# Kernel tuning notes

Measured on AMD Instinct MI355X. Metric: run time of the kernel, lower is better.

## Reference

```python
import jax, jax.numpy as jnp
import numpy as np

E, H, O = 64, 128, 16  # enc_hidden_dim, dec_hidden_dim, dec_output_dim (proj_size)
B, N, FUT = 64, 1000, 12


def _lstm_proj_cell(x, h, c, W_ih, W_hh, b_ih, b_hh, W_hr):
    # PyTorch gate order: input, forget, cell(g), output
    gates = x @ W_ih.T + h @ W_hh.T + (b_ih + b_hh)
    i, f, g, o = jnp.split(gates, 4, axis=-1)
    c_new = jax.nn.sigmoid(f) * c + jax.nn.sigmoid(i) * jnp.tanh(g)
    h_full = jax.nn.sigmoid(o) * jnp.tanh(c_new)
    h_new = h_full @ W_hr.T  # proj_size projection
    return h_new, c_new


def setup_inputs() -> dict:
    key = jax.random.key(0)
    ks = jax.random.split(key, 20)
    sc = 0.1
    inp = {
        "enc_outputs": jax.random.normal(ks[0], (B, 1, N, E), jnp.float32),
        "mean": jax.random.normal(ks[1], (B, FUT, N, O), jnp.float32),
        "s": jax.random.normal(ks[2], (1, O), jnp.float32),
        "h_0": jax.random.normal(ks[3], (2, O), jnp.float32),
        "c_0": jax.random.normal(ks[4], (2, H), jnp.float32),
        "W_ih_l0": sc * jax.random.normal(ks[5], (4 * H, E + O), jnp.float32),
        "W_hh_l0": sc * jax.random.normal(ks[6], (4 * H, O), jnp.float32),
        "b_ih_l0": sc * jax.random.normal(ks[7], (4 * H,), jnp.float32),
        "b_hh_l0": sc * jax.random.normal(ks[8], (4 * H,), jnp.float32),
        "W_hr_l0": sc * jax.random.normal(ks[9], (O, H), jnp.float32),
        "W_ih_l1": sc * jax.random.normal(ks[10], (4 * H, O), jnp.float32),
        "W_hh_l1": sc * jax.random.normal(ks[11], (4 * H, O), jnp.float32),
        "b_ih_l1": sc * jax.random.normal(ks[12], (4 * H,), jnp.float32),
        "b_hh_l1": sc * jax.random.normal(ks[13], (4 * H,), jnp.float32),
        "W_hr_l1": sc * jax.random.normal(ks[14], (O, H), jnp.float32),
        "future": FUT,
    }
    # forget-gate bias = 1.0 as in reset_bias()
    for nme in ("b_ih_l0", "b_hh_l0", "b_ih_l1", "b_hh_l1"):
        inp[nme] = inp[nme].at[H:2 * H].set(1.0)
    return inp


def _forward(enc_outputs, mean, s, h_0, c_0,
             W_ih_l0, W_hh_l0, b_ih_l0, b_hh_l0, W_hr_l0,
             W_ih_l1, W_hh_l1, b_ih_l1, b_hh_l1, W_hr_l1, future):
    b, _, n_nodes, _ = enc_outputs.shape
    enc = enc_outputs[:, 0]            # [B, N, E]
    node_mean = jnp.mean(mean, axis=1)  # [B, N, O]
    # state is carried across nodes AND timesteps: one chain of N*future steps
    node_idx = jnp.arange(n_nodes * future) // future

    last0 = jnp.broadcast_to(s[0], (b, s.shape[1]))
    h1_0 = jnp.broadcast_to(h_0[0], (b, h_0.shape[1]))
    h2_0 = jnp.broadcast_to(h_0[1], (b, h_0.shape[1]))
    c1_0 = jnp.broadcast_to(c_0[0], (b, c_0.shape[1]))
    c2_0 = jnp.broadcast_to(c_0[1], (b, c_0.shape[1]))

    def step(carry, n):
        last, h1, c1, h2, c2 = carry
        enc_t = jnp.take(enc, n, axis=1)        # [B, E]
        nm_t = jnp.take(node_mean, n, axis=1)   # [B, O]
        loop = last + nm_t                      # TFRate forced to 0.0 in source
        x = jnp.concatenate([enc_t, loop], axis=-1)
        h1, c1 = _lstm_proj_cell(x, h1, c1, W_ih_l0, W_hh_l0, b_ih_l0, b_hh_l0, W_hr_l0)
        h2, c2 = _lstm_proj_cell(h1, h2, c2, W_ih_l1, W_hh_l1, b_ih_l1, b_hh_l1, W_hr_l1)
        return (h2, h1, c1, h2, c2), h2 + nm_t

    _, outs = jax.lax.scan(step, (last0, h1_0, c1_0, h2_0, c2_0), node_idx)
    # outs: [N*future, B, O] -> [B, future, N, O]
    outs = outs.reshape(n_nodes, future, b, -1).transpose(2, 1, 0, 3)
    return outs


def reference(enc_outputs, mean, s, h_0, c_0,
              W_ih_l0, W_hh_l0, b_ih_l0, b_hh_l0, W_hr_l0,
              W_ih_l1, W_hh_l1, b_ih_l1, b_hh_l1, W_hr_l1, future):
    return _forward(enc_outputs, mean, s, h_0, c_0,
                    W_ih_l0, W_hh_l0, b_ih_l0, b_hh_l0, W_hr_l0,
                    W_ih_l1, W_hh_l1, b_ih_l1, b_hh_l1, W_hr_l1, future)
```

## Files before the change

kernel.cpp:

```cpp
#include <hip/hip_runtime.h>

#define BB 64
#define NN 1000
#define FF 12
#define EE 64
#define HH 128
#define OO 16

__device__ __forceinline__ float rcp_(float x){ return __builtin_amdgcn_rcpf(x); }
__device__ __forceinline__ float tanh_(float x){ return 1.0f - 2.0f*rcp_(__expf(2.0f*x) + 1.0f); }

template<int CTRL>
__device__ __forceinline__ float qswz_(float x){
    int r = __builtin_amdgcn_update_dpp(0, __float_as_int(x), CTRL, 0xF, 0xF, true);
    return __int_as_float(r);
}
__device__ __forceinline__ void barrier_lds_(){
    asm volatile("s_waitcnt lgkmcnt(0)" ::: "memory");
    __builtin_amdgcn_s_barrier();
    asm volatile("" ::: "memory");
}

__global__ __launch_bounds__(512, 1)
void decoder_kernel(const float* __restrict__ enc,
                    const float* __restrict__ mean,
                    const float* __restrict__ sv,
                    const float* __restrict__ h0,
                    const float* __restrict__ c0,
                    const float* __restrict__ Wih0,
                    const float* __restrict__ Whh0,
                    const float* __restrict__ bih0,
                    const float* __restrict__ bhh0,
                    const float* __restrict__ Whr0,
                    const float* __restrict__ Wih1,
                    const float* __restrict__ Whh1,
                    const float* __restrict__ bih1,
                    const float* __restrict__ bhh1,
                    const float* __restrict__ Whr1,
                    float* __restrict__ out)
{
    const int t   = threadIdx.x;
    const int b   = blockIdx.x;
    const int k   = t >> 2;
    const int tau = t & 3;
    const int g   = tau*HH + k;
    const int j16 = t >> 5;
    const int ln  = t & 31;
    const int kb  = ln * 4;

    __shared__ __align__(16) float s_h1[OO];
    __shared__ __align__(16) float s_h2[OO];
    __shared__ __align__(16) float s_hf[HH];
    __shared__ __align__(16) float s_enc[EE];
    __shared__ __align__(16) float s_nm[2][OO];

    float wl0[16], wh0[16], wi1[16], wh1[16], wp0[4], wp1[4];
    {
        const float4* pL = (const float4*)(Wih0 + (size_t)g*(EE+OO) + EE);
        const float4* pH = (const float4*)(Whh0 + (size_t)g*OO);
        const float4* pI = (const float4*)(Wih1 + (size_t)g*OO);
        const float4* pG = (const float4*)(Whh1 + (size_t)g*OO);
        #pragma unroll
        for (int i=0;i<4;i++){
            float4 v;
            v=pL[i]; wl0[4*i]=v.x; wl0[4*i+1]=v.y; wl0[4*i+2]=v.z; wl0[4*i+3]=v.w;
            v=pH[i]; wh0[4*i]=v.x; wh0[4*i+1]=v.y; wh0[4*i+2]=v.z; wh0[4*i+3]=v.w;
            v=pI[i]; wi1[4*i]=v.x; wi1[4*i+1]=v.y; wi1[4*i+2]=v.z; wi1[4*i+3]=v.w;
            v=pG[i]; wh1[4*i]=v.x; wh1[4*i+1]=v.y; wh1[4*i+2]=v.z; wh1[4*i+3]=v.w;
        }
        float4 q0 = *(const float4*)(Whr0 + (size_t)j16*HH + kb);
        float4 q1 = *(const float4*)(Whr1 + (size_t)j16*HH + kb);
        wp0[0]=q0.x; wp0[1]=q0.y; wp0[2]=q0.z; wp0[3]=q0.w;
        wp1[0]=q1.x; wp1[1]=q1.y; wp1[2]=q1.z; wp1[3]=q1.w;
    }
    const float bias0r = bih0[g] + bhh0[g];
    const float bias1r = bih1[g] + bhh1[g];
    float corr1 = 0.f;
    #pragma unroll
    for (int i=0;i<4;i++){
        float4 hv  = *(const float4*)(h0 + OO + 4*i);
        float4 svv = *(const float4*)(sv + 4*i);
        corr1 += (hv.x-svv.x)*wh1[4*i]   + (hv.y-svv.y)*wh1[4*i+1]
               + (hv.z-svv.z)*wh1[4*i+2] + (hv.w-svv.w)*wh1[4*i+3];
    }
    const float am = (tau==2) ? 2.0f : 1.0f;

    float c1v = c0[k];
    float c2v = c0[HH+k];

    const float* encB  = enc  + (size_t)b * NN * EE;
    const float* meanB = mean + (size_t)b * FF * NN * OO;
    float*       outB  = out  + (size_t)b * FF * NN * OO;

    if (t < OO){
        s_h1[t] = h0[t];
        s_h2[t] = sv[t];
        ((float4*)s_enc)[t] = ((const float4*)encB)[t];
    } else if (t < 2*OO){
        const int j = t - OO;
        float a = 0.f;
        #pragma unroll
        for (int ff=0; ff<FF; ++ff) a += meanB[((size_t)ff*NN)*OO + j];
        s_nm[0][j] = a * (1.0f/12.0f);
    }
    __syncthreads();

    float pre0;
    {
        float s = bias0r;
        const float4* wp = (const float4*)(Wih0 + (size_t)g*(EE+OO));
        const float4* ep = (const float4*)s_enc;
        #pragma unroll
        for (int e=0;e<16;e++){
            float4 wv = wp[e], ev = ep[e];
            s += ev.x*wv.x + ev.y*wv.y + ev.z*wv.z + ev.w*wv.w;
        }
        const float4* nm4 = (const float4*)s_nm[0];
        #pragma unroll
        for (int i=0;i<4;i++){
            float4 m = nm4[i];
            s += m.x*wl0[4*i] + m.y*wl0[4*i+1] + m.z*wl0[4*i+2] + m.w*wl0[4*i+3];
        }
        pre0 = s;
    }

    float4 ef = make_float4(0.f,0.f,0.f,0.f);
    float nmr[12];
    #pragma unroll
    for (int i=0;i<12;i++) nmr[i]=0.f;

    for (int n = 0; n < NN; ++n){
        for (int f = 0; f < FF; ++f){
            float h2v[16];
            float aL, aH;
            {
                const float4* pa = (const float4*)s_h2;
                const float4* pb = (const float4*)s_h1;
                float x0=0,x1=0,x2=0,x3=0, y0=0,y1=0,y2=0,y3=0;
                #pragma unroll
                for (int i=0;i<4;i++){
                    float4 a = pa[i];
                    h2v[4*i]=a.x; h2v[4*i+1]=a.y; h2v[4*i+2]=a.z; h2v[4*i+3]=a.w;
                    x0 += a.x*wl0[4*i]; x1 += a.y*wl0[4*i+1];
                    x2 += a.z*wl0[4*i+2]; x3 += a.w*wl0[4*i+3];
                    float4 c = pb[i];
                    y0 += c.x*wh0[4*i]; y1 += c.y*wh0[4*i+1];
                    y2 += c.z*wh0[4*i+2]; y3 += c.w*wh0[4*i+3];
                }
                aL = (x0+x1)+(x2+x3);
                aH = (y0+y1)+(y2+y3);
            }
            float xg  = pre0 + aL + aH;
            float act = 1.f - am * rcp_(__expf(am*xg) + 1.f);

            float r2 = qswz_<0x4E>(act);
            float P  = act * r2;
            float s2 = (tau==1) ? act*c1v : P;
            float cn = s2 + qswz_<0xB1>(s2);
            c1v = cn;
            float tc = tanh_(cn);
            float hf = act * qswz_<0x4E>(tc);
            if (tau == 3) s_hf[k] = hf;
            barrier_lds_();

            {
                float4 h4 = *(const float4*)&s_hf[kb];
                float p = h4.x*wp0[0] + h4.y*wp0[1] + h4.z*wp0[2] + h4.w*wp0[3];
                p += __shfl_down(p, 16, 32);
                p += __shfl_down(p,  8, 32);
                p += __shfl_down(p,  4, 32);
                p += __shfl_down(p,  2, 32);
                p += __shfl_down(p,  1, 32);
                if (ln == 0) s_h1[j16] = p;
            }
            barrier_lds_();

            float aI, aH2;
            {
                const float4* pa = (const float4*)s_h1;
                float x0=0,x1=0,x2=0,x3=0, y0=0,y1=0,y2=0,y3=0;
                #pragma unroll
                for (int i=0;i<4;i++){
                    float4 a = pa[i];
                    x0 += a.x*wi1[4*i];   x1 += a.y*wi1[4*i+1];
                    x2 += a.z*wi1[4*i+2]; x3 += a.w*wi1[4*i+3];
                    y0 += h2v[4*i]  *wh1[4*i];   y1 += h2v[4*i+1]*wh1[4*i+1];
                    y2 += h2v[4*i+2]*wh1[4*i+2]; y3 += h2v[4*i+3]*wh1[4*i+3];
                }
                aI  = (x0+x1)+(x2+x3);
                aH2 = (y0+y1)+(y2+y3);
            }
            float xg1 = bias1r + aI + aH2;
            if (n == 0 && f == 0) xg1 += corr1;
            float act1 = 1.f - am * rcp_(__expf(am*xg1) + 1.f);

            float r2b = qswz_<0x4E>(act1);
            float Pb  = act1 * r2b;
            float s2b = (tau==1) ? act1*c2v : Pb;
            float cnb = s2b + qswz_<0xB1>(s2b);
            c2v = cnb;
            float tcb = tanh_(cnb);
            float hf2 = act1 * qswz_<0x4E>(tcb);
            if (tau == 3) s_hf[k] = hf2;

            if (f == 8 && n+1 < NN){
                if (t < OO){
                    ef = ((const float4*)(encB + (size_t)(n+1)*EE))[t];
                } else if (t < 2*OO){
                    const int j = t - OO;
                    #pragma unroll
                    for (int ff=0; ff<FF; ++ff) nmr[ff] = meanB[((size_t)ff*NN + (n+1))*OO + j];
                }
            }
            if (f == 10 && n+1 < NN){
                if (t < OO){
                    ((float4*)s_enc)[t] = ef;
                } else if (t < 2*OO){
                    float a = 0.f;
                    #pragma unroll
                    for (int ff=0; ff<FF; ++ff) a += nmr[ff];
                    s_nm[(n+1)&1][t-OO] = a * (1.0f/12.0f);
                }
            }
            barrier_lds_();

            {
                float4 h4 = *(const float4*)&s_hf[kb];
                float p = h4.x*wp1[0] + h4.y*wp1[1] + h4.z*wp1[2] + h4.w*wp1[3];
                p += __shfl_down(p, 16, 32);
                p += __shfl_down(p,  8, 32);
                p += __shfl_down(p,  4, 32);
                p += __shfl_down(p,  2, 32);
                p += __shfl_down(p,  1, 32);
                if (ln == 0){
                    s_h2[j16] = p;
                    outB[((size_t)f*NN + n)*OO + j16] = p + s_nm[n&1][j16];
                }
            }
            if (f == 11 && n+1 < NN){
                float s = bias0r;
                const float4* wp = (const float4*)(Wih0 + (size_t)g*(EE+OO));
                const float4* ep = (const float4*)s_enc;
                #pragma unroll
                for (int e=0;e<16;e++){
                    float4 wv = wp[e], ev = ep[e];
                    s += ev.x*wv.x + ev.y*wv.y + ev.z*wv.z + ev.w*wv.w;
                }
                const float4* nm4 = (const float4*)s_nm[(n+1)&1];
                #pragma unroll
                for (int i=0;i<4;i++){
                    float4 m = nm4[i];
                    s += m.x*wl0[4*i] + m.y*wl0[4*i+1] + m.z*wl0[4*i+2] + m.w*wl0[4*i+3];
                }
                pre0 = s;
            }
            barrier_lds_();
        }
    }
}

extern "C" void kernel_launch(void* const* d_in, const int* in_sizes, int n_in,
                              void* d_out, int out_size, void* d_ws, size_t ws_size,
                              hipStream_t stream) {
    const float* enc  = (const float*)d_in[0];
    const float* mean = (const float*)d_in[1];
    const float* sv   = (const float*)d_in[2];
    const float* h0   = (const float*)d_in[3];
    const float* c0   = (const float*)d_in[4];
    const float* Wih0 = (const float*)d_in[5];
    const float* Whh0 = (const float*)d_in[6];
    const float* bih0 = (const float*)d_in[7];
    const float* bhh0 = (const float*)d_in[8];
    const float* Whr0 = (const float*)d_in[9];
    const float* Wih1 = (const float*)d_in[10];
    const float* Whh1 = (const float*)d_in[11];
    const float* bih1 = (const float*)d_in[12];
    const float* bhh1 = (const float*)d_in[13];
    const float* Whr1 = (const float*)d_in[14];
    float* out = (float*)d_out;

    decoder_kernel<<<dim3(BB), dim3(512), 0, stream>>>(
        enc, mean, sv, h0, c0,
        Wih0, Whh0, bih0, bhh0, Whr0,
        Wih1, Whh1, bih1, bhh1, Whr1,
        out);
}
```

Baseline: 18.01 ms.

## Replace DPP quad gate exchange with LDS gate staging and extra barriers

Each thread now computes one gate row indexed directly by thread id, writes the activated gate to shared memory, and the first 128 threads then combine i/f/g/o to update the cell state. This replaces the DPP quad-swizzle layout, where four lanes holding one hidden unit's gates exchanged values in registers. The change adds two block-wide barriers per cell step and LDS round trips on the serial recurrence path, and leaves three quarters of the threads idle during the cell update. It also raises the launch-bounds occupancy hint to two blocks per CU and keeps separate last/h2 buffers instead of the initial-step correction term.

```diff
diff --git a/kernel.cpp b/kernel.cpp
--- a/kernel.cpp
+++ b/kernel.cpp
@@ -6,22 +6,18 @@
 #define EE 64
 #define HH 128
 #define OO 16
+#define GG 512
 
 __device__ __forceinline__ float rcp_(float x){ return __builtin_amdgcn_rcpf(x); }
 __device__ __forceinline__ float tanh_(float x){ return 1.0f - 2.0f*rcp_(__expf(2.0f*x) + 1.0f); }
 
-template<int CTRL>
-__device__ __forceinline__ float qswz_(float x){
-    int r = __builtin_amdgcn_update_dpp(0, __float_as_int(x), CTRL, 0xF, 0xF, true);
-    return __int_as_float(r);
-}
 __device__ __forceinline__ void barrier_lds_(){
     asm volatile("s_waitcnt lgkmcnt(0)" ::: "memory");
     __builtin_amdgcn_s_barrier();
     asm volatile("" ::: "memory");
 }
 
-__global__ __launch_bounds__(512, 1)
+__global__ __launch_bounds__(512, 2)
 void decoder_kernel(const float* __restrict__ enc,
                     const float* __restrict__ mean,
                     const float* __restrict__ sv,
@@ -39,66 +35,60 @@
                     const float* __restrict__ Whr1,
                     float* __restrict__ out)
 {
-    const int t   = threadIdx.x;
-    const int b   = blockIdx.x;
-    const int k   = t >> 2;
-    const int tau = t & 3;
-    const int g   = tau*HH + k;
-    const int j16 = t >> 5;
-    const int ln  = t & 31;
-    const int kb  = ln * 4;
-
+    const int t = threadIdx.x;
+    const int b = blockIdx.x;
+
+    __shared__ __align__(16) float s_last[OO];
     __shared__ __align__(16) float s_h1[OO];
     __shared__ __align__(16) float s_h2[OO];
-    __shared__ __align__(16) float s_hf[HH];
+    __shared__ __align__(16) float s_gates[GG];
+    __shared__ __align__(16) float s_hfull[HH];
     __shared__ __align__(16) float s_enc[EE];
     __shared__ __align__(16) float s_nm[2][OO];
 
-    float wl0[16], wh0[16], wi1[16], wh1[16], wp0[4], wp1[4];
+    float w_loop[16], w_hh0[16], w_ih1[16], w_hh1[16], wp0[4], wp1[4];
     {
-        const float4* pL = (const float4*)(Wih0 + (size_t)g*(EE+OO) + EE);
-        const float4* pH = (const float4*)(Whh0 + (size_t)g*OO);
-        const float4* pI = (const float4*)(Wih1 + (size_t)g*OO);
-        const float4* pG = (const float4*)(Whh1 + (size_t)g*OO);
+        const float4* pL = (const float4*)(Wih0 + (size_t)t*(EE+OO) + EE);
+        const float4* pH = (const float4*)(Whh0 + (size_t)t*OO);
+        const float4* pI = (const float4*)(Wih1 + (size_t)t*OO);
+        const float4* pG = (const float4*)(Whh1 + (size_t)t*OO);
         #pragma unroll
         for (int i=0;i<4;i++){
             float4 v;
-            v=pL[i]; wl0[4*i]=v.x; wl0[4*i+1]=v.y; wl0[4*i+2]=v.z; wl0[4*i+3]=v.w;
-            v=pH[i]; wh0[4*i]=v.x; wh0[4*i+1]=v.y; wh0[4*i+2]=v.z; wh0[4*i+3]=v.w;
-            v=pI[i]; wi1[4*i]=v.x; wi1[4*i+1]=v.y; wi1[4*i+2]=v.z; wi1[4*i+3]=v.w;
-            v=pG[i]; wh1[4*i]=v.x; wh1[4*i+1]=v.y; wh1[4*i+2]=v.z; wh1[4*i+3]=v.w;
-        }
+            v=pL[i]; w_loop[4*i]=v.x; w_loop[4*i+1]=v.y; w_loop[4*i+2]=v.z; w_loop[4*i+3]=v.w;
+            v=pH[i]; w_hh0[4*i]=v.x; w_hh0[4*i+1]=v.y; w_hh0[4*i+2]=v.z; w_hh0[4*i+3]=v.w;
+            v=pI[i]; w_ih1[4*i]=v.x; w_ih1[4*i+1]=v.y; w_ih1[4*i+2]=v.z; w_ih1[4*i+3]=v.w;
+            v=pG[i]; w_hh1[4*i]=v.x; w_hh1[4*i+1]=v.y; w_hh1[4*i+2]=v.z; w_hh1[4*i+3]=v.w;
+        }
+    }
+    const float bias0 = bih0[t] + bhh0[t];
+    const float bias1 = bih1[t] + bhh1[t];
+    const float am = ((t >> 7) == 2) ? 2.0f : 1.0f;
+
+    const int j16 = t >> 5;
+    const int kb  = (t & 31) * 4;
+    {
         float4 q0 = *(const float4*)(Whr0 + (size_t)j16*HH + kb);
         float4 q1 = *(const float4*)(Whr1 + (size_t)j16*HH + kb);
         wp0[0]=q0.x; wp0[1]=q0.y; wp0[2]=q0.z; wp0[3]=q0.w;
         wp1[0]=q1.x; wp1[1]=q1.y; wp1[2]=q1.z; wp1[3]=q1.w;
     }
-    const float bias0r = bih0[g] + bhh0[g];
-    const float bias1r = bih1[g] + bhh1[g];
-    float corr1 = 0.f;
-    #pragma unroll
-    for (int i=0;i<4;i++){
-        float4 hv  = *(const float4*)(h0 + OO + 4*i);
-        float4 svv = *(const float4*)(sv + 4*i);
-        corr1 += (hv.x-svv.x)*wh1[4*i]   + (hv.y-svv.y)*wh1[4*i+1]
-               + (hv.z-svv.z)*wh1[4*i+2] + (hv.w-svv.w)*wh1[4*i+3];
-    }
-    const float am = (tau==2) ? 2.0f : 1.0f;
-
-    float c1v = c0[k];
-    float c2v = c0[HH+k];
+
+    float c1 = (t < HH) ? c0[t]      : 0.0f;
+    float c2 = (t < HH) ? c0[HH + t] : 0.0f;
 
     const float* encB  = enc  + (size_t)b * NN * EE;
     const float* meanB = mean + (size_t)b * FF * NN * OO;
     float*       outB  = out  + (size_t)b * FF * NN * OO;
 
     if (t < OO){
-        s_h1[t] = h0[t];
-        s_h2[t] = sv[t];
+        s_last[t] = sv[t];
+        s_h1[t]   = h0[t];
+        s_h2[t]   = h0[OO + t];
         ((float4*)s_enc)[t] = ((const float4*)encB)[t];
     } else if (t < 2*OO){
         const int j = t - OO;
-        float a = 0.f;
+        float a = 0.0f;
         #pragma unroll
         for (int ff=0; ff<FF; ++ff) a += meanB[((size_t)ff*NN)*OO + j];
         s_nm[0][j] = a * (1.0f/12.0f);
@@ -107,8 +97,8 @@
 
     float pre0;
     {
-        float s = bias0r;
-        const float4* wp = (const float4*)(Wih0 + (size_t)g*(EE+OO));
+        float s = bias0;
+        const float4* wp = (const float4*)(Wih0 + (size_t)t*(EE+OO));
         const float4* ep = (const float4*)s_enc;
         #pragma unroll
         for (int e=0;e<16;e++){
@@ -119,7 +109,7 @@
         #pragma unroll
         for (int i=0;i<4;i++){
             float4 m = nm4[i];
-            s += m.x*wl0[4*i] + m.y*wl0[4*i+1] + m.z*wl0[4*i+2] + m.w*wl0[4*i+3];
+            s += m.x*w_loop[4*i] + m.y*w_loop[4*i+1] + m.z*w_loop[4*i+2] + m.w*w_loop[4*i+3];
         }
         pre0 = s;
     }
@@ -131,78 +121,62 @@
 
     for (int n = 0; n < NN; ++n){
         for (int f = 0; f < FF; ++f){
-            float h2v[16];
-            float aL, aH;
-            {
-                const float4* pa = (const float4*)s_h2;
+            {
+                float acc = pre0;
+                const float4* pa = (const float4*)s_last;
                 const float4* pb = (const float4*)s_h1;
                 float x0=0,x1=0,x2=0,x3=0, y0=0,y1=0,y2=0,y3=0;
                 #pragma unroll
                 for (int i=0;i<4;i++){
                     float4 a = pa[i];
-                    h2v[4*i]=a.x; h2v[4*i+1]=a.y; h2v[4*i+2]=a.z; h2v[4*i+3]=a.w;
-                    x0 += a.x*wl0[4*i]; x1 += a.y*wl0[4*i+1];
-                    x2 += a.z*wl0[4*i+2]; x3 += a.w*wl0[4*i+3];
+                    x0 += a.x*w_loop[4*i];   x1 += a.y*w_loop[4*i+1];
+                    x2 += a.z*w_loop[4*i+2]; x3 += a.w*w_loop[4*i+3];
                     float4 c = pb[i];
-                    y0 += c.x*wh0[4*i]; y1 += c.y*wh0[4*i+1];
-                    y2 += c.z*wh0[4*i+2]; y3 += c.w*wh0[4*i+3];
-                }
-                aL = (x0+x1)+(x2+x3);
-                aH = (y0+y1)+(y2+y3);
-            }
-            float xg  = pre0 + aL + aH;
-            float act = 1.f - am * rcp_(__expf(am*xg) + 1.f);
-
-            float r2 = qswz_<0x4E>(act);
-            float P  = act * r2;
-            float s2 = (tau==1) ? act*c1v : P;
-            float cn = s2 + qswz_<0xB1>(s2);
-            c1v = cn;
-            float tc = tanh_(cn);
-            float hf = act * qswz_<0x4E>(tc);
-            if (tau == 3) s_hf[k] = hf;
-            barrier_lds_();
-
-            {
-                float4 h4 = *(const float4*)&s_hf[kb];
+                    y0 += c.x*w_hh0[4*i];   y1 += c.y*w_hh0[4*i+1];
+                    y2 += c.z*w_hh0[4*i+2]; y3 += c.w*w_hh0[4*i+3];
+                }
+                acc += (x0+x1)+(x2+x3) + (y0+y1)+(y2+y3);
+                s_gates[t] = 1.f - am * rcp_(__expf(am*acc) + 1.f);
+            }
+            barrier_lds_();
+
+            if (t < HH){
+                float iv = s_gates[t],      fv = s_gates[HH + t];
+                float gv = s_gates[2*HH+t], ov = s_gates[3*HH + t];
+                c1 = fv*c1 + iv*gv;
+                s_hfull[t] = ov * tanh_(c1);
+            }
+            barrier_lds_();
+
+            {
+                float4 h4 = *(const float4*)&s_hfull[kb];
                 float p = h4.x*wp0[0] + h4.y*wp0[1] + h4.z*wp0[2] + h4.w*wp0[3];
                 p += __shfl_down(p, 16, 32);
                 p += __shfl_down(p,  8, 32);
                 p += __shfl_down(p,  4, 32);
                 p += __shfl_down(p,  2, 32);
                 p += __shfl_down(p,  1, 32);
-                if (ln == 0) s_h1[j16] = p;
-            }
-            barrier_lds_();
-
-            float aI, aH2;
-            {
+                if ((t & 31) == 0) s_h1[j16] = p;
+            }
+            barrier_lds_();
+
+            {
+                float acc1 = bias1;
                 const float4* pa = (const float4*)s_h1;
+                const float4* pb = (const float4*)s_h2;
                 float x0=0,x1=0,x2=0,x3=0, y0=0,y1=0,y2=0,y3=0;
                 #pragma unroll
                 for (int i=0;i<4;i++){
                     float4 a = pa[i];
-                    x0 += a.x*wi1[4*i];   x1 += a.y*wi1[4*i+1];
-                    x2 += a.z*wi1[4*i+2]; x3 += a.w*wi1[4*i+3];
-                    y0 += h2v[4*i]  *wh1[4*i];   y1 += h2v[4*i+1]*wh1[4*i+1];
-                    y2 += h2v[4*i+2]*wh1[4*i+2]; y3 += h2v[4*i+3]*wh1[4*i+3];
-                }
-                aI  = (x0+x1)+(x2+x3);
-                aH2 = (y0+y1)+(y2+y3);
-            }
-            float xg1 = bias1r + aI + aH2;
-            if (n == 0 && f == 0) xg1 += corr1;
-            float act1 = 1.f - am * rcp_(__expf(am*xg1) + 1.f);
-
-            float r2b = qswz_<0x4E>(act1);
-            float Pb  = act1 * r2b;
-            float s2b = (tau==1) ? act1*c2v : Pb;
-            float cnb = s2b + qswz_<0xB1>(s2b);
-            c2v = cnb;
-            float tcb = tanh_(cnb);
-            float hf2 = act1 * qswz_<0x4E>(tcb);
-            if (tau == 3) s_hf[k] = hf2;
-
+                    x0 += a.x*w_ih1[4*i];   x1 += a.y*w_ih1[4*i+1];
+                    x2 += a.z*w_ih1[4*i+2]; x3 += a.w*w_ih1[4*i+3];
+                    float4 c = pb[i];
+                    y0 += c.x*w_hh1[4*i];   y1 += c.y*w_hh1[4*i+1];
+                    y2 += c.z*w_hh1[4*i+2]; y3 += c.w*w_hh1[4*i+3];
+                }
+                acc1 += (x0+x1)+(x2+x3) + (y0+y1)+(y2+y3);
+                s_gates[t] = 1.f - am * rcp_(__expf(am*acc1) + 1.f);
+            }
             if (f == 8 && n+1 < NN){
                 if (t < OO){
                     ef = ((const float4*)(encB + (size_t)(n+1)*EE))[t];
@@ -224,22 +198,31 @@
             }
             barrier_lds_();
 
-            {
-                float4 h4 = *(const float4*)&s_hf[kb];
+            if (t < HH){
+                float iv = s_gates[t],      fv = s_gates[HH + t];
+                float gv = s_gates[2*HH+t], ov = s_gates[3*HH + t];
+                c2 = fv*c2 + iv*gv;
+                s_hfull[t] = ov * tanh_(c2);
+            }
+            barrier_lds_();
+
+            {
+                float4 h4 = *(const float4*)&s_hfull[kb];
                 float p = h4.x*wp1[0] + h4.y*wp1[1] + h4.z*wp1[2] + h4.w*wp1[3];
                 p += __shfl_down(p, 16, 32);
                 p += __shfl_down(p,  8, 32);
                 p += __shfl_down(p,  4, 32);
                 p += __shfl_down(p,  2, 32);
                 p += __shfl_down(p,  1, 32);
-                if (ln == 0){
-                    s_h2[j16] = p;
+                if ((t & 31) == 0){
+                    s_h2[j16]   = p;
+                    s_last[j16] = p;
                     outB[((size_t)f*NN + n)*OO + j16] = p + s_nm[n&1][j16];
                 }
             }
             if (f == 11 && n+1 < NN){
-                float s = bias0r;
-                const float4* wp = (const float4*)(Wih0 + (size_t)g*(EE+OO));
+                float s = bias0;
+                const float4* wp = (const float4*)(Wih0 + (size_t)t*(EE+OO));
                 const float4* ep = (const float4*)s_enc;
                 #pragma unroll
                 for (int e=0;e<16;e++){
@@ -250,7 +233,7 @@
                 #pragma unroll
                 for (int i=0;i<4;i++){
                     float4 m = nm4[i];
-                    s += m.x*wl0[4*i] + m.y*wl0[4*i+1] + m.z*wl0[4*i+2] + m.w*wl0[4*i+3];
+                    s += m.x*w_loop[4*i] + m.y*w_loop[4*i+1] + m.z*w_loop[4*i+2] + m.w*w_loop[4*i+3];
                 }
                 pre0 = s;
             }
```

Result: slower. 20.22 ms (+12.3%).
